# Performance work log

Hardware: AMD Instinct MI355X
Metric: run time of the kernel (lower is better)

The kernel has to match this reference:

```python
import jax, jax.numpy as jnp
import numpy as np
import math

D_MODEL = 1024
NUM_HEADS = 16
DIM_FF = 4096
B, N = 4, 1024
GRID = 32
R_LEFT = 1.0
R_RIGHT = 1.0
LN_EPS = 1e-5


def get_alibi_slopes(n_heads):
    def pow2(n):
        start = 2 ** (-2 ** (-(math.log2(n) - 3)))
        return [start * start ** i for i in range(n)]
    if math.log2(n_heads).is_integer():
        slopes = pow2(n_heads)
    else:
        m = 2 ** math.floor(math.log2(n_heads))
        slopes = pow2(m)
        slopes += [slopes[-1] * 0.5 ** (i + 1) for i in range(n_heads - m)]
    return jnp.asarray(np.array(slopes, dtype=np.float32))


def setup_inputs() -> dict:
    key = jax.random.key(0)
    ks = jax.random.split(key, 16)
    s = 1.0 / math.sqrt(D_MODEL)
    inp = {
        "src": jax.random.normal(ks[0], (B, N, D_MODEL), jnp.float32),
        "coords": jax.random.randint(ks[1], (B, N, 2), 0, GRID, jnp.int32),
        "Wq": jax.random.normal(ks[2], (D_MODEL, D_MODEL), jnp.float32) * s,
        "Wk": jax.random.normal(ks[3], (D_MODEL, D_MODEL), jnp.float32) * s,
        "Wv": jax.random.normal(ks[4], (D_MODEL, D_MODEL), jnp.float32) * s,
        "Wo": jax.random.normal(ks[5], (D_MODEL, D_MODEL), jnp.float32) * s,
        "W1": jax.random.normal(ks[6], (DIM_FF, D_MODEL), jnp.float32) * s,
        "b1": jnp.zeros((DIM_FF,), jnp.float32),
        "W2": jax.random.normal(ks[7], (D_MODEL, DIM_FF), jnp.float32) * (1.0 / math.sqrt(DIM_FF)),
        "b2": jnp.zeros((D_MODEL,), jnp.float32),
        "g1": jnp.ones((D_MODEL,), jnp.float32),
        "be1": jnp.zeros((D_MODEL,), jnp.float32),
        "g2": jnp.ones((D_MODEL,), jnp.float32),
        "be2": jnp.zeros((D_MODEL,), jnp.float32),
    }
    return inp


def layer_norm(x, g, b):
    mu = jnp.mean(x, axis=-1, keepdims=True)
    var = jnp.mean(jnp.square(x - mu), axis=-1, keepdims=True)
    return (x - mu) * jax.lax.rsqrt(var + LN_EPS) * g + b


def alibi_2d_bias(coords, slopes):
    # coords: (B, N, 2) int -> bias (B, H, N, N)
    x = coords[..., 0].astype(jnp.float32)
    y = coords[..., 1].astype(jnp.float32)
    dist = jnp.abs(x[:, :, None] - x[:, None, :]) + jnp.abs(y[:, :, None] - y[:, None, :])
    flat = y * (x.max() + 1.0) + x  # global x.max(), matching torch code
    le = (flat[:, None, :] <= flat[:, :, None]).astype(jnp.float32)  # (B,N,N)
    s = slopes.reshape(1, -1, 1, 1)
    left = s * R_LEFT
    right = s * R_RIGHT
    return dist[:, None] * (le[:, None] * left + (1.0 - le[:, None]) * right)


def reference(src, coords, Wq, Wk, Wv, Wo, W1, b1, W2, b2, g1, be1, g2, be2):
    H, Hd = NUM_HEADS, D_MODEL // NUM_HEADS
    scale = Hd ** (-0.5)
    slopes = get_alibi_slopes(H)
    bias = alibi_2d_bias(coords, slopes)  # (B,H,N,N)

    Bn, Nn, D = src.shape
    q = (src @ Wq.T).reshape(Bn, Nn, H, Hd)
    k = (src @ Wk.T).reshape(Bn, Nn, H, Hd)
    v = (src @ Wv.T).reshape(Bn, Nn, H, Hd)
    attn = jnp.einsum("bnhd,bmhd->bhnm", q, k) * scale + bias
    attn = jax.nn.softmax(attn, axis=-1)
    out = jnp.einsum("bhnm,bmhd->bnhd", attn, v).reshape(Bn, Nn, D)
    src2 = out @ Wo.T

    x = layer_norm(src + src2, g1, be1)
    ff = (jax.nn.gelu(x @ W1.T + b1, approximate=False)) @ W2.T + b2
    return layer_norm(x + ff, g2, be2)
```

## Files before the change

kernel.cpp:

```cpp
#include <hip/hip_runtime.h>
#include <hip/hip_bf16.h>
#include <math.h>

#define DEV __device__ __forceinline__

typedef __attribute__((ext_vector_type(4))) float f32x4;
typedef __attribute__((ext_vector_type(8))) short bf16x8;
typedef __attribute__((ext_vector_type(4))) unsigned short us4;

DEV unsigned short f2bf(float f) {
    union { float f; unsigned u; } v; v.f = f;
    unsigned r = v.u + 0x7FFF + ((v.u >> 16) & 1);
    return (unsigned short)(r >> 16);
}

DEV void async16(const void* g, void* l) {
    __builtin_amdgcn_global_load_lds(
        (const __attribute__((address_space(1))) void*)g,
        (__attribute__((address_space(3))) void*)l, 16, 0, 0);
}

__global__ void cvt_kernel(const float* __restrict__ in, unsigned short* __restrict__ out, int n4) {
    int i = blockIdx.x * blockDim.x + threadIdx.x;
    if (i >= n4) return;
    f32x4 v = ((const f32x4*)in)[i];
    us4 o;
    o.x = f2bf(v.x); o.y = f2bf(v.y); o.z = f2bf(v.z); o.w = f2bf(v.w);
    ((us4*)out)[i] = o;
}

#define BM 128
#define BN 128
#define BKK 64

template<int EPI>
__global__ __launch_bounds__(256) void gemm_bt(
    const unsigned short* __restrict__ A,
    const unsigned short* __restrict__ B,
    float* __restrict__ Cf, unsigned short* __restrict__ Cb,
    const float* __restrict__ bias,
    int M, int N, int K)
{
    __shared__ unsigned short As[BM * BKK];
    __shared__ unsigned short Bs[BN * BKK];

    const int tid  = threadIdx.x;
    const int wid  = tid >> 6, lane = tid & 63;
    const int l15  = lane & 15, l16 = lane >> 4;
    const int wr   = wid >> 1, wc = wid & 1;
    const int row0 = blockIdx.y * BM;
    const int col0 = blockIdx.x * BN;

    f32x4 acc[4][4] = {};

    const int nkt = K / BKK;
    for (int kt = 0; kt < nkt; ++kt) {
        const int k0 = kt * BKK;
        __syncthreads();
#pragma unroll
        for (int i = 0; i < 4; ++i) {
            int c = i * 256 + tid;
            int row = c >> 3, slot = c & 7;
            int ks = (slot ^ (row & 7)) * 8;
            async16(A + (size_t)(row0 + row) * K + k0 + ks, (char*)As + c * 16);
            async16(B + (size_t)(col0 + row) * K + k0 + ks, (char*)Bs + c * 16);
        }
        __syncthreads();
#pragma unroll
        for (int kk = 0; kk < 2; ++kk) {
            bf16x8 af[4], bfr[4];
#pragma unroll
            for (int m = 0; m < 4; ++m) {
                int r = wr * 64 + m * 16 + l15;
                int slot = (kk * 4 + l16) ^ (r & 7);
                af[m] = *(const bf16x8*)((const char*)As + r * 128 + slot * 16);
            }
#pragma unroll
            for (int n = 0; n < 4; ++n) {
                int r = wc * 64 + n * 16 + l15;
                int slot = (kk * 4 + l16) ^ (r & 7);
                bfr[n] = *(const bf16x8*)((const char*)Bs + r * 128 + slot * 16);
            }
#pragma unroll
            for (int m = 0; m < 4; ++m)
#pragma unroll
                for (int n = 0; n < 4; ++n)
                    acc[m][n] = __builtin_amdgcn_mfma_f32_16x16x32_bf16(af[m], bfr[n], acc[m][n], 0, 0, 0);
        }
    }

#pragma unroll
    for (int m = 0; m < 4; ++m) {
        int grow = row0 + wr * 64 + m * 16 + l16 * 4;
#pragma unroll
        for (int n = 0; n < 4; ++n) {
            int gcol = col0 + wc * 64 + n * 16 + l15;
            float bv = (EPI >= 2) ? bias[gcol] : 0.f;
#pragma unroll
            for (int r = 0; r < 4; ++r) {
                float v = acc[m][n][r];
                size_t idx = (size_t)(grow + r) * N + gcol;
                if (EPI == 0) {
                    Cb[idx] = f2bf(v);
                } else if (EPI == 1) {
                    Cf[idx] = v;
                } else if (EPI == 2) {
                    v += bv;
                    v = 0.5f * v * (1.f + erff(v * 0.70710678118f));
                    Cb[idx] = f2bf(v);
                } else {
                    Cf[idx] = v + bv;
                }
            }
        }
    }
}

__global__ __launch_bounds__(256) void transpose_v(const unsigned short* __restrict__ qkv,
                                                   unsigned short* __restrict__ vt)
{
    __shared__ unsigned short t[64][72];
    const int n0 = blockIdx.x * 64;
    const int bh = blockIdx.y;
    const int b = bh >> 4, h = bh & 15;
    const int tid = threadIdx.x;
#pragma unroll
    for (int i = 0; i < 2; ++i) {
        int c = i * 256 + tid;
        int row = c >> 3, col0 = (c & 7) * 8;
        const unsigned short* src = qkv + (size_t)(b * 1024 + n0 + row) * 3072 + 2048 + h * 64 + col0;
        bf16x8 v = *(const bf16x8*)src;
#pragma unroll
        for (int j = 0; j < 8; ++j) t[row][col0 + j] = (unsigned short)v[j];
    }
    __syncthreads();
#pragma unroll
    for (int i = 0; i < 2; ++i) {
        int c = i * 256 + tid;
        int hd = c >> 3, col0 = (c & 7) * 8;
        bf16x8 v;
#pragma unroll
        for (int j = 0; j < 8; ++j) v[j] = (short)t[col0 + j][hd];
        *(bf16x8*)(vt + ((size_t)bh * 64 + hd) * 1024 + n0 + col0) = v;
    }
}

__global__ __launch_bounds__(256) void attn_kernel(const unsigned short* __restrict__ qkv,
                                                   const int* __restrict__ coords,
                                                   const unsigned short* __restrict__ vt,
                                                   unsigned short* __restrict__ out)
{
    __shared__ unsigned short Ks[2][64 * 64];
    __shared__ unsigned short Vs[2][64 * 64];
    __shared__ unsigned short P[4][16][80];

    const int tid = threadIdx.x, wid = tid >> 6, lane = tid & 63;
    const int l15 = lane & 15, l16 = lane >> 4;
    const int q0 = blockIdx.x * 64;
    const int bh = blockIdx.y;
    const int b = bh >> 4, h = bh & 15;
    const float slope = exp2f(-0.5f * (float)(h + 1));
    const float scale = 0.125f;

    const int c0 = tid,        r0c = c0 >> 3, ks0 = ((c0 & 7) ^ (r0c & 7)) * 8;
    const int c1 = 256 + tid,  r1c = c1 >> 3, ks1 = ((c1 & 7) ^ (r1c & 7)) * 8;
    const unsigned short* kbase = qkv + (size_t)(b * 1024) * 3072 + 1024 + h * 64;
    const unsigned short* vbase = vt + (size_t)bh * 64 * 1024;

    bf16x8 qf[2];
    {
        const unsigned short* qp = qkv + (size_t)(b * 1024 + q0 + wid * 16 + l15) * 3072 + h * 64 + l16 * 8;
        qf[0] = *(const bf16x8*)qp;
        qf[1] = *(const bf16x8*)(qp + 32);
    }
    float qx[4], qy[4];
#pragma unroll
    for (int r = 0; r < 4; ++r) {
        int qr = q0 + wid * 16 + l16 * 4 + r;
        int2 c = ((const int2*)coords)[b * 1024 + qr];
        qx[r] = (float)c.x; qy[r] = (float)c.y;
    }

    float mr[4], lr[4];
    f32x4 o[4] = {};
#pragma unroll
    for (int r = 0; r < 4; ++r) { mr[r] = -1e30f; lr[r] = 0.f; }

    {
        async16(kbase + (size_t)r0c * 3072 + ks0, (char*)Ks[0] + c0 * 16);
        async16(kbase + (size_t)r1c * 3072 + ks1, (char*)Ks[0] + c1 * 16);
        async16(vbase + (size_t)r0c * 1024 + ks0, (char*)Vs[0] + c0 * 16);
        async16(vbase + (size_t)r1c * 1024 + ks1, (char*)Vs[0] + c1 * 16);
    }
    int cur = 0;

    for (int t = 0; t < 16; ++t) {
        const int kv0 = t * 64;
        __syncthreads();
        if (t < 15) {
            const int kv1 = kv0 + 64;
            async16(kbase + (size_t)(kv1 + r0c) * 3072 + ks0, (char*)Ks[cur ^ 1] + c0 * 16);
            async16(kbase + (size_t)(kv1 + r1c) * 3072 + ks1, (char*)Ks[cur ^ 1] + c1 * 16);
            async16(vbase + (size_t)r0c * 1024 + kv1 + ks0, (char*)Vs[cur ^ 1] + c0 * 16);
            async16(vbase + (size_t)r1c * 1024 + kv1 + ks1, (char*)Vs[cur ^ 1] + c1 * 16);
        }
        int2 kc[4];
#pragma unroll
        for (int ct = 0; ct < 4; ++ct)
            kc[ct] = ((const int2*)coords)[b * 1024 + kv0 + ct * 16 + l15];

        f32x4 s[4] = {};
        __builtin_amdgcn_s_setprio(1);
#pragma unroll
        for (int kk = 0; kk < 2; ++kk) {
#pragma unroll
            for (int ct = 0; ct < 4; ++ct) {
                int r = ct * 16 + l15;
                int slot = (kk * 4 + l16) ^ (r & 7);
                bf16x8 kf = *(const bf16x8*)((const char*)Ks[cur] + r * 128 + slot * 16);
                s[ct] = __builtin_amdgcn_mfma_f32_16x16x32_bf16(qf[kk], kf, s[ct], 0, 0, 0);
            }
        }
        __builtin_amdgcn_s_setprio(0);

#pragma unroll
        for (int ct = 0; ct < 4; ++ct) {
            float kx = (float)kc[ct].x, ky = (float)kc[ct].y;
#pragma unroll
            for (int r = 0; r < 4; ++r) {
                float d = fabsf(qx[r] - kx) + fabsf(qy[r] - ky);
                s[ct][r] = s[ct][r] * scale + slope * d;
            }
        }
#pragma unroll
        for (int r = 0; r < 4; ++r) {
            float mx = fmaxf(fmaxf(s[0][r], s[1][r]), fmaxf(s[2][r], s[3][r]));
#pragma unroll
            for (int off = 1; off < 16; off <<= 1) mx = fmaxf(mx, __shfl_xor(mx, off, 64));
            float mn = fmaxf(mr[r], mx);
            float corr = __expf(mr[r] - mn);
            mr[r] = mn;
            float sum = 0.f;
#pragma unroll
            for (int ct = 0; ct < 4; ++ct) {
                float p = __expf(s[ct][r] - mn);
                s[ct][r] = p;
                sum += p;
            }
#pragma unroll
            for (int off = 1; off < 16; off <<= 1) sum += __shfl_xor(sum, off, 64);
            lr[r] = lr[r] * corr + sum;
#pragma unroll
            for (int ht = 0; ht < 4; ++ht) o[ht][r] *= corr;
        }
#pragma unroll
        for (int ct = 0; ct < 4; ++ct)
#pragma unroll
            for (int r = 0; r < 4; ++r)
                P[wid][l16 * 4 + r][ct * 16 + l15] = f2bf(s[ct][r]);

        __builtin_amdgcn_s_setprio(1);
#pragma unroll
        for (int kk = 0; kk < 2; ++kk) {
            bf16x8 pa = *(const bf16x8*)&P[wid][l15][kk * 32 + l16 * 8];
#pragma unroll
            for (int ht = 0; ht < 4; ++ht) {
                int rv = ht * 16 + l15;
                int slot = (kk * 4 + l16) ^ (rv & 7);
                bf16x8 vf = *(const bf16x8*)((const char*)Vs[cur] + rv * 128 + slot * 16);
                o[ht] = __builtin_amdgcn_mfma_f32_16x16x32_bf16(pa, vf, o[ht], 0, 0, 0);
            }
        }
        __builtin_amdgcn_s_setprio(0);
        cur ^= 1;
    }
#pragma unroll
    for (int ht = 0; ht < 4; ++ht)
#pragma unroll
        for (int r = 0; r < 4; ++r) {
            size_t idx = (size_t)(b * 1024 + q0 + wid * 16 + l16 * 4 + r) * 1024 + h * 64 + ht * 16 + l15;
            out[idx] = f2bf(o[ht][r] / lr[r]);
        }
}

__global__ __launch_bounds__(256) void ln_kernel(const float* __restrict__ a, const float* __restrict__ bres,
                                                 const float* __restrict__ g, const float* __restrict__ be,
                                                 float* __restrict__ xout, unsigned short* __restrict__ xb)
{
    __shared__ float red[2][4];
    const int row = blockIdx.x, tid = threadIdx.x;
    const int wid = tid >> 6, lane = tid & 63;
    f32x4 v = ((const f32x4*)a)[(size_t)row * 256 + tid] + ((const f32x4*)bres)[(size_t)row * 256 + tid];
    float s1 = v.x + v.y + v.z + v.w;
    float s2 = v.x * v.x + v.y * v.y + v.z * v.z + v.w * v.w;
#pragma unroll
    for (int off = 1; off < 64; off <<= 1) {
        s1 += __shfl_xor(s1, off, 64);
        s2 += __shfl_xor(s2, off, 64);
    }
    if (lane == 0) { red[0][wid] = s1; red[1][wid] = s2; }
    __syncthreads();
    s1 = red[0][0] + red[0][1] + red[0][2] + red[0][3];
    s2 = red[1][0] + red[1][1] + red[1][2] + red[1][3];
    float mu = s1 * (1.f / 1024.f);
    float var = s2 * (1.f / 1024.f) - mu * mu;
    float rstd = rsqrtf(var + 1e-5f);
    f32x4 gv = ((const f32x4*)g)[tid], bev = ((const f32x4*)be)[tid];
    f32x4 y = (v - mu) * rstd * gv + bev;
    if (xout) ((f32x4*)xout)[(size_t)row * 256 + tid] = y;
    if (xb) {
        us4 ob;
        ob.x = f2bf(y.x); ob.y = f2bf(y.y); ob.z = f2bf(y.z); ob.w = f2bf(y.w);
        ((us4*)xb)[(size_t)row * 256 + tid] = ob;
    }
}

extern "C" void kernel_launch(void* const* d_in, const int* in_sizes, int n_in,
                              void* d_out, int out_size, void* d_ws, size_t ws_size,
                              hipStream_t stream) {
    const float* src    = (const float*)d_in[0];
    const int*   coords = (const int*)d_in[1];
    const float* Wq     = (const float*)d_in[2];
    const float* Wk     = (const float*)d_in[3];
    const float* Wv     = (const float*)d_in[4];
    const float* Wo     = (const float*)d_in[5];
    const float* W1     = (const float*)d_in[6];
    const float* b1     = (const float*)d_in[7];
    const float* W2     = (const float*)d_in[8];
    const float* b2     = (const float*)d_in[9];
    const float* g1     = (const float*)d_in[10];
    const float* be1    = (const float*)d_in[11];
    const float* g2     = (const float*)d_in[12];
    const float* be2    = (const float*)d_in[13];
    float* out = (float*)d_out;

    char* ws = (char*)d_ws;
    size_t off = 0;
    auto alloc = [&](size_t bytes) { size_t o = off; off += (bytes + 255) & ~(size_t)255; return o; };

    const size_t BT = 4096;
    size_t qkv_off   = alloc(BT * 3072 * 2);
    size_t attno_off = alloc(BT * 1024 * 2);
    size_t vt_off    = alloc((size_t)64 * 64 * 1024 * 2);
    size_t regionA_end = off;
    size_t x_off    = alloc(BT * 1024 * 4);
    size_t ffs_off  = alloc(BT * 1024 * 4);
    size_t srcb_off = alloc(BT * 1024 * 2);
    size_t wqkv_off = alloc((size_t)3072 * 1024 * 2);
    size_t wo_off   = alloc((size_t)1024 * 1024 * 2);
    size_t w1_off   = alloc((size_t)4096 * 1024 * 2);
    size_t w2_off   = alloc((size_t)1024 * 4096 * 2);
    (void)regionA_end; (void)ws_size; (void)in_sizes; (void)n_in; (void)out_size;

    unsigned short* qkv   = (unsigned short*)(ws + qkv_off);
    unsigned short* attno = (unsigned short*)(ws + attno_off);
    unsigned short* vt    = (unsigned short*)(ws + vt_off);
    float*          x     = (float*)(ws + x_off);
    float*          src2  = (float*)(ws + ffs_off);
    float*          ff    = (float*)(ws + ffs_off);
    unsigned short* srcb  = (unsigned short*)(ws + srcb_off);
    unsigned short* xb    = (unsigned short*)(ws + srcb_off);
    unsigned short* wqkvb = (unsigned short*)(ws + wqkv_off);
    unsigned short* wob   = (unsigned short*)(ws + wo_off);
    unsigned short* w1b   = (unsigned short*)(ws + w1_off);
    unsigned short* w2b   = (unsigned short*)(ws + w2_off);
    unsigned short* h1    = (unsigned short*)(ws + qkv_off);

    auto cvt = [&](const float* in, unsigned short* o, size_t n) {
        int n4 = (int)(n / 4);
        cvt_kernel<<<(n4 + 255) / 256, 256, 0, stream>>>(in, o, n4);
    };
    cvt(src, srcb, BT * 1024);
    cvt(Wq, wqkvb, 1024 * 1024);
    cvt(Wk, wqkvb + 1024 * 1024, 1024 * 1024);
    cvt(Wv, wqkvb + 2 * 1024 * 1024, 1024 * 1024);
    cvt(Wo, wob, 1024 * 1024);
    cvt(W1, w1b, 4096 * 1024);
    cvt(W2, w2b, 1024 * 4096);

    gemm_bt<0><<<dim3(3072 / BN, 4096 / BM), 256, 0, stream>>>(srcb, wqkvb, nullptr, qkv, nullptr, 4096, 3072, 1024);
    transpose_v<<<dim3(16, 64), 256, 0, stream>>>(qkv, vt);
    attn_kernel<<<dim3(16, 64), 256, 0, stream>>>(qkv, coords, vt, attno);
    gemm_bt<1><<<dim3(1024 / BN, 4096 / BM), 256, 0, stream>>>(attno, wob, src2, nullptr, nullptr, 4096, 1024, 1024);
    ln_kernel<<<4096, 256, 0, stream>>>(src, src2, g1, be1, x, xb);
    gemm_bt<2><<<dim3(4096 / BN, 4096 / BM), 256, 0, stream>>>(xb, w1b, nullptr, h1, b1, 4096, 4096, 1024);
    gemm_bt<3><<<dim3(1024 / BN, 4096 / BM), 256, 0, stream>>>(h1, w2b, ff, nullptr, b2, 4096, 1024, 4096);
    ln_kernel<<<4096, 256, 0, stream>>>(x, ff, g2, be2, out, nullptr);
}
```

Baseline: 417.4 us.

## Rewrite attention with 32x32 transposed MFMA, register-resident P, lazy rescale

```diff
diff --git a/kernel.cpp b/kernel.cpp
--- a/kernel.cpp
+++ b/kernel.cpp
@@ -5,6 +5,7 @@
 #define DEV __device__ __forceinline__
 
 typedef __attribute__((ext_vector_type(4))) float f32x4;
+typedef __attribute__((ext_vector_type(16))) float f32x16;
 typedef __attribute__((ext_vector_type(8))) short bf16x8;
 typedef __attribute__((ext_vector_type(4))) unsigned short us4;
 
@@ -152,46 +153,55 @@
 {
     __shared__ unsigned short Ks[2][64 * 64];
     __shared__ unsigned short Vs[2][64 * 64];
-    __shared__ unsigned short P[4][16][80];
+    __shared__ float cF[1024 * 2];
 
     const int tid = threadIdx.x, wid = tid >> 6, lane = tid & 63;
-    const int l15 = lane & 15, l16 = lane >> 4;
-    const int q0 = blockIdx.x * 64;
+    const int l31 = lane & 31, hi = lane >> 5;
+    const int q0 = blockIdx.x * 128;
     const int bh = blockIdx.y;
     const int b = bh >> 4, h = bh & 15;
-    const float slope = exp2f(-0.5f * (float)(h + 1));
-    const float scale = 0.125f;
-
-    const int c0 = tid,        r0c = c0 >> 3, ks0 = ((c0 & 7) ^ (r0c & 7)) * 8;
-    const int c1 = 256 + tid,  r1c = c1 >> 3, ks1 = ((c1 & 7) ^ (r1c & 7)) * 8;
+    const float LOG2E = 1.4426950408889634f;
+    const float slope2 = exp2f(-0.5f * (float)(h + 1)) * LOG2E;
+    const float scale2 = 0.125f * LOG2E;
+
+    const int c0 = tid,       r0c = c0 >> 3, ks0 = ((c0 & 7) ^ (r0c & 7)) * 8;
+    const int c1 = 256 + tid, r1c = c1 >> 3, ks1 = ((c1 & 7) ^ (r1c & 7)) * 8;
     const unsigned short* kbase = qkv + (size_t)(b * 1024) * 3072 + 1024 + h * 64;
     const unsigned short* vbase = vt + (size_t)bh * 64 * 1024;
 
-    bf16x8 qf[2];
     {
-        const unsigned short* qp = qkv + (size_t)(b * 1024 + q0 + wid * 16 + l15) * 3072 + h * 64 + l16 * 8;
+        const int2* cp = (const int2*)coords + b * 1024;
+#pragma unroll
+        for (int i = 0; i < 4; ++i) {
+            int kv = i * 256 + tid;
+            int2 c = cp[kv];
+            cF[kv * 2]     = slope2 * (float)c.x;
+            cF[kv * 2 + 1] = slope2 * (float)c.y;
+        }
+    }
+
+    const int qrow = q0 + wid * 32 + l31;
+    bf16x8 qf[4];
+    {
+        const unsigned short* qp = qkv + (size_t)(b * 1024 + qrow) * 3072 + h * 64 + hi * 8;
         qf[0] = *(const bf16x8*)qp;
-        qf[1] = *(const bf16x8*)(qp + 32);
-    }
-    float qx[4], qy[4];
-#pragma unroll
-    for (int r = 0; r < 4; ++r) {
-        int qr = q0 + wid * 16 + l16 * 4 + r;
-        int2 c = ((const int2*)coords)[b * 1024 + qr];
-        qx[r] = (float)c.x; qy[r] = (float)c.y;
-    }
-
-    float mr[4], lr[4];
-    f32x4 o[4] = {};
-#pragma unroll
-    for (int r = 0; r < 4; ++r) { mr[r] = -1e30f; lr[r] = 0.f; }
-
+        qf[1] = *(const bf16x8*)(qp + 16);
+        qf[2] = *(const bf16x8*)(qp + 32);
+        qf[3] = *(const bf16x8*)(qp + 48);
+    }
+    float qxs, qys;
     {
-        async16(kbase + (size_t)r0c * 3072 + ks0, (char*)Ks[0] + c0 * 16);
-        async16(kbase + (size_t)r1c * 3072 + ks1, (char*)Ks[0] + c1 * 16);
-        async16(vbase + (size_t)r0c * 1024 + ks0, (char*)Vs[0] + c0 * 16);
-        async16(vbase + (size_t)r1c * 1024 + ks1, (char*)Vs[0] + c1 * 16);
-    }
+        int2 qc = ((const int2*)coords)[b * 1024 + qrow];
+        qxs = slope2 * (float)qc.x; qys = slope2 * (float)qc.y;
+    }
+
+    float mr = -1e30f, lr = 0.f;
+    f32x16 o0 = (f32x16)0.f, o1 = (f32x16)0.f;
+
+    async16(kbase + (size_t)r0c * 3072 + ks0, (char*)Ks[0] + c0 * 16);
+    async16(kbase + (size_t)r1c * 3072 + ks1, (char*)Ks[0] + c1 * 16);
+    async16(vbase + (size_t)r0c * 1024 + ks0, (char*)Vs[0] + c0 * 16);
+    async16(vbase + (size_t)r1c * 1024 + ks1, (char*)Vs[0] + c1 * 16);
     int cur = 0;
 
     for (int t = 0; t < 16; ++t) {
@@ -204,83 +214,101 @@
             async16(vbase + (size_t)r0c * 1024 + kv1 + ks0, (char*)Vs[cur ^ 1] + c0 * 16);
             async16(vbase + (size_t)r1c * 1024 + kv1 + ks1, (char*)Vs[cur ^ 1] + c1 * 16);
         }
-        int2 kc[4];
-#pragma unroll
-        for (int ct = 0; ct < 4; ++ct)
-            kc[ct] = ((const int2*)coords)[b * 1024 + kv0 + ct * 16 + l15];
-
-        f32x4 s[4] = {};
+
+        f32x16 s0 = (f32x16)0.f, s1 = (f32x16)0.f;
         __builtin_amdgcn_s_setprio(1);
 #pragma unroll
-        for (int kk = 0; kk < 2; ++kk) {
-#pragma unroll
-            for (int ct = 0; ct < 4; ++ct) {
-                int r = ct * 16 + l15;
-                int slot = (kk * 4 + l16) ^ (r & 7);
-                bf16x8 kf = *(const bf16x8*)((const char*)Ks[cur] + r * 128 + slot * 16);
-                s[ct] = __builtin_amdgcn_mfma_f32_16x16x32_bf16(qf[kk], kf, s[ct], 0, 0, 0);
+        for (int c16 = 0; c16 < 4; ++c16) {
+            int slot = ((c16 * 2 + hi) ^ (l31 & 7)) * 16;
+            bf16x8 k0f = *(const bf16x8*)((const char*)Ks[cur] + l31 * 128 + slot);
+            bf16x8 k1f = *(const bf16x8*)((const char*)Ks[cur] + (32 + l31) * 128 + slot);
+            s0 = __builtin_amdgcn_mfma_f32_32x32x16_bf16(k0f, qf[c16], s0, 0, 0, 0);
+            s1 = __builtin_amdgcn_mfma_f32_32x32x16_bf16(k1f, qf[c16], s1, 0, 0, 0);
+        }
+        __builtin_amdgcn_s_setprio(0);
+
+#pragma unroll
+        for (int T = 0; T < 2; ++T) {
+            f32x16& S = T ? s1 : s0;
+#pragma unroll
+            for (int u = 0; u < 4; ++u) {
+                int kvb = kv0 + T * 32 + u * 8 + hi * 4;
+                f32x4 ca = *(const f32x4*)&cF[kvb * 2];
+                f32x4 cb = *(const f32x4*)&cF[kvb * 2 + 4];
+                S[4*u+0] = S[4*u+0] * scale2 + (fabsf(qxs - ca.x) + fabsf(qys - ca.y));
+                S[4*u+1] = S[4*u+1] * scale2 + (fabsf(qxs - ca.z) + fabsf(qys - ca.w));
+                S[4*u+2] = S[4*u+2] * scale2 + (fabsf(qxs - cb.x) + fabsf(qys - cb.y));
+                S[4*u+3] = S[4*u+3] * scale2 + (fabsf(qxs - cb.z) + fabsf(qys - cb.w));
             }
         }
-        __builtin_amdgcn_s_setprio(0);
-
-#pragma unroll
-        for (int ct = 0; ct < 4; ++ct) {
-            float kx = (float)kc[ct].x, ky = (float)kc[ct].y;
-#pragma unroll
-            for (int r = 0; r < 4; ++r) {
-                float d = fabsf(qx[r] - kx) + fabsf(qy[r] - ky);
-                s[ct][r] = s[ct][r] * scale + slope * d;
-            }
-        }
-#pragma unroll
-        for (int r = 0; r < 4; ++r) {
-            float mx = fmaxf(fmaxf(s[0][r], s[1][r]), fmaxf(s[2][r], s[3][r]));
-#pragma unroll
-            for (int off = 1; off < 16; off <<= 1) mx = fmaxf(mx, __shfl_xor(mx, off, 64));
-            float mn = fmaxf(mr[r], mx);
-            float corr = __expf(mr[r] - mn);
-            mr[r] = mn;
-            float sum = 0.f;
-#pragma unroll
-            for (int ct = 0; ct < 4; ++ct) {
-                float p = __expf(s[ct][r] - mn);
-                s[ct][r] = p;
-                sum += p;
-            }
-#pragma unroll
-            for (int off = 1; off < 16; off <<= 1) sum += __shfl_xor(sum, off, 64);
-            lr[r] = lr[r] * corr + sum;
-#pragma unroll
-            for (int ht = 0; ht < 4; ++ht) o[ht][r] *= corr;
-        }
-#pragma unroll
-        for (int ct = 0; ct < 4; ++ct)
-#pragma unroll
-            for (int r = 0; r < 4; ++r)
-                P[wid][l16 * 4 + r][ct * 16 + l15] = f2bf(s[ct][r]);
+
+        float pm = s0[0];
+#pragma unroll
+        for (int i = 1; i < 16; ++i) pm = fmaxf(pm, s0[i]);
+#pragma unroll
+        for (int i = 0; i < 16; ++i) pm = fmaxf(pm, s1[i]);
+        pm = fmaxf(pm, __shfl_xor(pm, 32, 64));
+        if (__any(pm > mr + 8.0f)) {
+            float mn = fmaxf(mr, pm);
+            float corr = exp2f(mr - mn);
+            mr = mn;
+            lr *= corr;
+#pragma unroll
+            for (int i = 0; i < 16; ++i) { o0[i] *= corr; o1[i] *= corr; }
+        }
+        float sum = 0.f;
+#pragma unroll
+        for (int i = 0; i < 16; ++i) { float p = exp2f(s0[i] - mr); s0[i] = p; sum += p; }
+#pragma unroll
+        for (int i = 0; i < 16; ++i) { float p = exp2f(s1[i] - mr); s1[i] = p; sum += p; }
+        sum += __shfl_xor(sum, 32, 64);
+        lr += sum;
+
+        bf16x8 pf[4];
+#pragma unroll
+        for (int c = 0; c < 4; ++c) {
+            const f32x16& S = (c < 2) ? s0 : s1;
+            const int e = (c & 1) * 8;
+            unsigned x0, x1, y0, y1;
+            asm("v_cvt_pk_bf16_f32 %0, %1, %2" : "=v"(x0) : "v"(S[e+0]), "v"(S[e+1]));
+            asm("v_cvt_pk_bf16_f32 %0, %1, %2" : "=v"(x1) : "v"(S[e+2]), "v"(S[e+3]));
+            asm("v_cvt_pk_bf16_f32 %0, %1, %2" : "=v"(y0) : "v"(S[e+4]), "v"(S[e+5]));
+            asm("v_cvt_pk_bf16_f32 %0, %1, %2" : "=v"(y1) : "v"(S[e+6]), "v"(S[e+7]));
+            asm("v_permlane32_swap_b32 %0, %1" : "+v"(x0), "+v"(y0));
+            asm("v_permlane32_swap_b32 %0, %1" : "+v"(x1), "+v"(y1));
+            union { unsigned u[4]; bf16x8 v; } pk_;
+            pk_.u[0] = x0; pk_.u[1] = x1; pk_.u[2] = y0; pk_.u[3] = y1;
+            pf[c] = pk_.v;
+        }
 
         __builtin_amdgcn_s_setprio(1);
 #pragma unroll
-        for (int kk = 0; kk < 2; ++kk) {
-            bf16x8 pa = *(const bf16x8*)&P[wid][l15][kk * 32 + l16 * 8];
-#pragma unroll
-            for (int ht = 0; ht < 4; ++ht) {
-                int rv = ht * 16 + l15;
-                int slot = (kk * 4 + l16) ^ (rv & 7);
-                bf16x8 vf = *(const bf16x8*)((const char*)Vs[cur] + rv * 128 + slot * 16);
-                o[ht] = __builtin_amdgcn_mfma_f32_16x16x32_bf16(pa, vf, o[ht], 0, 0, 0);
-            }
+        for (int c = 0; c < 4; ++c) {
+            int slot = ((c * 2 + hi) ^ (l31 & 7)) * 16;
+            bf16x8 v0 = *(const bf16x8*)((const char*)Vs[cur] + l31 * 128 + slot);
+            bf16x8 v1 = *(const bf16x8*)((const char*)Vs[cur] + (32 + l31) * 128 + slot);
+            o0 = __builtin_amdgcn_mfma_f32_32x32x16_bf16(v0, pf[c], o0, 0, 0, 0);
+            o1 = __builtin_amdgcn_mfma_f32_32x32x16_bf16(v1, pf[c], o1, 0, 0, 0);
         }
         __builtin_amdgcn_s_setprio(0);
         cur ^= 1;
     }
-#pragma unroll
-    for (int ht = 0; ht < 4; ++ht)
-#pragma unroll
-        for (int r = 0; r < 4; ++r) {
-            size_t idx = (size_t)(b * 1024 + q0 + wid * 16 + l16 * 4 + r) * 1024 + h * 64 + ht * 16 + l15;
-            out[idx] = f2bf(o[ht][r] / lr[r]);
-        }
+
+    const float inv = 1.0f / lr;
+    unsigned short* op = out + (size_t)(b * 1024 + qrow) * 1024 + h * 64;
+#pragma unroll
+    for (int Td = 0; Td < 2; ++Td) {
+        const f32x16& O = Td ? o1 : o0;
+#pragma unroll
+        for (int u = 0; u < 4; ++u) {
+            us4 w;
+            w.x = f2bf(O[4*u+0] * inv);
+            w.y = f2bf(O[4*u+1] * inv);
+            w.z = f2bf(O[4*u+2] * inv);
+            w.w = f2bf(O[4*u+3] * inv);
+            *(us4*)(op + Td * 32 + u * 8 + hi * 4) = w;
+        }
+    }
 }
 
 __global__ __launch_bounds__(256) void ln_kernel(const float* __restrict__ a, const float* __restrict__ bres,
@@ -380,7 +408,7 @@
 
     gemm_bt<0><<<dim3(3072 / BN, 4096 / BM), 256, 0, stream>>>(srcb, wqkvb, nullptr, qkv, nullptr, 4096, 3072, 1024);
     transpose_v<<<dim3(16, 64), 256, 0, stream>>>(qkv, vt);
-    attn_kernel<<<dim3(16, 64), 256, 0, stream>>>(qkv, coords, vt, attno);
+    attn_kernel<<<dim3(8, 64), 256, 0, stream>>>(qkv, coords, vt, attno);
     gemm_bt<1><<<dim3(1024 / BN, 4096 / BM), 256, 0, stream>>>(attno, wob, src2, nullptr, nullptr, 4096, 1024, 1024);
     ln_kernel<<<4096, 256, 0, stream>>>(src, src2, g1, be1, x, xb);
     gemm_bt<2><<<dim3(4096 / BN, 4096 / BM), 256, 0, stream>>>(xb, w1b, nullptr, h1, b1, 4096, 4096, 1024);
```

After: 403.2 us. 1.04x faster.
